# Optimization experiments

Hardware: AMD Instinct MI355X
Metric: run time of the kernel (lower is better)

Reference implementation:

```python
import jax, jax.numpy as jnp
import numpy as np

N_NODES = 20000
N_FEAT = 10
EDGE_DIM = 6
D = 256
H = 8
C = D // H  # 32 per-head channels for gat1/gat2
B = 2048
E = 320000
NEG = 0.2        # LeakyReLU slope in GATConv attention
BN_EPS = 1e-5


def _bn_eval(x, g, b):
    # BatchNorm1d in eval mode with fresh buffers: running_mean=0, running_var=1
    return g * x * (1.0 / np.sqrt(1.0 + BN_EPS)) + b


def _gat(x, src, dst, edge_attr, W, a_src, a_dst, We, a_e, bias, heads, out_ch, n):
    # PyG GATConv with edge_dim: shared src/dst linear, per-head additive attention
    xp = (x @ W).reshape(n, heads, out_ch)                       # [N,H,C]
    al_s = jnp.einsum('nhc,hc->nh', xp, a_src)                   # [N,H]
    al_d = jnp.einsum('nhc,hc->nh', xp, a_dst)                   # [N,H]
    ep = (edge_attr @ We).reshape(-1, heads, out_ch)             # [E,H,C]
    al_e = jnp.einsum('ehc,hc->eh', ep, a_e)                     # [E,H]
    alpha = jax.nn.leaky_relu(al_s[src] + al_d[dst] + al_e, NEG)  # [E,H]
    # segment softmax over incoming edges of each dst node
    amax = jax.ops.segment_max(alpha, dst, num_segments=n)
    amax = jnp.where(jnp.isfinite(amax), amax, 0.0)
    ex = jnp.exp(alpha - amax[dst])
    den = jax.ops.segment_sum(ex, dst, num_segments=n)
    w = ex / (den[dst] + 1e-16)
    out = jax.ops.segment_sum(xp[src] * w[..., None], dst, num_segments=n)
    return out.reshape(n, heads * out_ch) + bias


def setup_inputs():
    key = jax.random.key(0)
    ks = iter(jax.random.split(key, 40))
    def rn(shape, scale=0.05):
        return jax.random.normal(next(ks), shape, dtype=jnp.float32) * scale
    inp = {}
    inp['current_node_ids'] = jax.random.randint(next(ks), (B,), 0, N_NODES)
    inp['network_features'] = jax.random.normal(next(ks), (B, N_FEAT), dtype=jnp.float32)
    inp['edge_index'] = jax.random.randint(next(ks), (2, E), 0, N_NODES)
    inp['edge_attr'] = jax.random.normal(next(ks), (E, EDGE_DIM), dtype=jnp.float32)
    inp['emb'] = rn((N_NODES, D), 1.0)
    inp['net_w1'] = rn((N_FEAT, D)); inp['net_b1'] = jnp.zeros((D,), jnp.float32)
    inp['net_g1'] = jnp.ones((D,), jnp.float32); inp['net_be1'] = jnp.zeros((D,), jnp.float32)
    inp['net_w2'] = rn((D, D)); inp['net_b2'] = jnp.zeros((D,), jnp.float32)
    inp['net_g2'] = jnp.ones((D,), jnp.float32); inp['net_be2'] = jnp.zeros((D,), jnp.float32)
    for i, (h, c) in enumerate([(H, C), (H, C), (1, D)], start=1):
        inp[f'gat{i}_W'] = rn((D, h * c))
        inp[f'gat{i}_as'] = rn((h, c)); inp[f'gat{i}_ad'] = rn((h, c))
        inp[f'gat{i}_We'] = rn((EDGE_DIM, h * c)); inp[f'gat{i}_ae'] = rn((h, c))
        inp[f'gat{i}_b'] = jnp.zeros((h * c,), jnp.float32)
    inp['fus_w'] = rn((2 * D, D)); inp['fus_b'] = jnp.zeros((D,), jnp.float32)
    inp['fus_g'] = jnp.ones((D,), jnp.float32); inp['fus_be'] = jnp.zeros((D,), jnp.float32)
    inp['cls_w'] = rn((D, N_NODES)); inp['cls_b'] = jnp.zeros((N_NODES,), jnp.float32)
    return inp


def reference(current_node_ids, network_features, edge_index, edge_attr, emb,
              net_w1, net_b1, net_g1, net_be1, net_w2, net_b2, net_g2, net_be2,
              gat1_W, gat1_as, gat1_ad, gat1_We, gat1_ae, gat1_b,
              gat2_W, gat2_as, gat2_ad, gat2_We, gat2_ae, gat2_b,
              gat3_W, gat3_as, gat3_ad, gat3_We, gat3_ae, gat3_b,
              fus_w, fus_b, fus_g, fus_be, cls_w, cls_b):
    src, dst = edge_index[0], edge_index[1]
    n = emb.shape[0]
    x = jax.nn.relu(_gat(emb, src, dst, edge_attr, gat1_W, gat1_as, gat1_ad, gat1_We, gat1_ae, gat1_b, H, C, n))
    x = jax.nn.relu(_gat(x, src, dst, edge_attr, gat2_W, gat2_as, gat2_ad, gat2_We, gat2_ae, gat2_b, H, C, n))
    x = _gat(x, src, dst, edge_attr, gat3_W, gat3_as, gat3_ad, gat3_We, gat3_ae, gat3_b, 1, D, n)
    node_emb = x[current_node_ids]                               # [B,D]
    h1 = jax.nn.relu(_bn_eval(network_features @ net_w1 + net_b1, net_g1, net_be1))
    net_emb = jax.nn.relu(_bn_eval(h1 @ net_w2 + net_b2, net_g2, net_be2))
    combined = jnp.concatenate([node_emb, net_emb], axis=1)      # [B,2D]
    fused = jax.nn.relu(_bn_eval(combined @ fus_w + fus_b, fus_g, fus_be))
    return fused @ cls_w + cls_b                                 # [B, N_NODES]
```

## Files before the change

kernel.cpp:

```cpp
#include <hip/hip_runtime.h>

#define NEG_SLOPE 0.2f
static constexpr float BN_INV = 0.9999950000374997f;

typedef __bf16 bf16x8 __attribute__((ext_vector_type(8)));
typedef float  f32x4  __attribute__((ext_vector_type(4)));

__device__ inline float4 bf4f(ushort4 u){
  float4 r;
  r.x = __uint_as_float((unsigned)u.x << 16);
  r.y = __uint_as_float((unsigned)u.y << 16);
  r.z = __uint_as_float((unsigned)u.z << 16);
  r.w = __uint_as_float((unsigned)u.w << 16);
  return r;
}
__device__ inline ushort4 f4bf(float4 v){
  ushort4 u;
  u.x = __builtin_bit_cast(unsigned short, (__bf16)v.x);
  u.y = __builtin_bit_cast(unsigned short, (__bf16)v.y);
  u.z = __builtin_bit_cast(unsigned short, (__bf16)v.z);
  u.w = __builtin_bit_cast(unsigned short, (__bf16)v.w);
  return u;
}

__global__ void hist_kernel(const int* __restrict__ dst, int* __restrict__ cnt, int E){
  int e = blockIdx.x*256 + threadIdx.x;
  if (e < E) atomicAdd(&cnt[dst[e]], 1);
}

__global__ __launch_bounds__(1024) void scan_kernel(int* __restrict__ cnt_cursor, int* __restrict__ offs, int n){
  __shared__ int wsum[16];
  int tid = threadIdx.x, lane = tid & 63, wv = tid >> 6;
  if (tid == 0) offs[0] = 0;
  int carry = 0;
  for (int base = 0; base < n; base += 1024){
    int i = base + tid;
    int v = (i < n) ? cnt_cursor[i] : 0;
    int x = v;
#pragma unroll
    for (int off = 1; off < 64; off <<= 1){
      int t = __shfl_up(x, off);
      if (lane >= off) x += t;
    }
    if (lane == 63) wsum[wv] = x;
    __syncthreads();
    int y = (lane < 16) ? wsum[lane] : 0;
#pragma unroll
    for (int off = 1; off < 16; off <<= 1){
      int t = __shfl_up(y, off);
      if (lane >= off) y += t;
    }
    int excl  = (wv == 0) ? 0 : __shfl(y, wv - 1);
    int total = __shfl(y, 15);
    int inc = carry + excl + x;
    if (i < n){ offs[i+1] = inc; cnt_cursor[i] = inc - v; }
    carry += total;
    __syncthreads();
  }
}

__global__ void scatter_kernel(const int* __restrict__ src, const int* __restrict__ dst,
                               const float* __restrict__ ea, int* __restrict__ cursor,
                               int* __restrict__ perm_src, int* __restrict__ perm_dst,
                               float* __restrict__ ea_perm, int E){
  int e = blockIdx.x*256 + threadIdx.x;
  if (e >= E) return;
  int d = dst[e];
  int pos = atomicAdd(&cursor[d], 1);
  perm_src[pos] = src[e];
  perm_dst[pos] = d;
#pragma unroll
  for (int k = 0; k < 6; ++k) ea_perm[(size_t)pos*6 + k] = ea[(size_t)e*6 + k];
}

__global__ void foldm_all_kernel(const float* __restrict__ We1, const float* __restrict__ ae1,
                                 const float* __restrict__ We2, const float* __restrict__ ae2,
                                 const float* __restrict__ We3, const float* __restrict__ ae3,
                                 float* __restrict__ M){
  int t = threadIdx.x;
  if (t < 96){
    const float* We = (t < 48) ? We1 : We2;
    const float* ae = (t < 48) ? ae1 : ae2;
    int u = t % 48, k = u / 8, h = u % 8;
    float s = 0.f;
    for (int c = 0; c < 32; ++c) s += We[k*256 + h*32 + c] * ae[h*32 + c];
    M[t] = s;
  } else if (t < 102){
    int k = t - 96;
    float s = 0.f;
    for (int c = 0; c < 256; ++c) s += We3[k*256 + c] * ae3[c];
    M[t] = s;
  }
}

template<bool USE_BIAS, bool USE_BN, bool USE_RELU, typename OutT>
__global__ __launch_bounds__(256) void gemm_kernel(
    const float* __restrict__ A, const float* __restrict__ W,
    const float* __restrict__ bias, const float* __restrict__ gam, const float* __restrict__ bet,
    OutT* __restrict__ C, int M, int N, int K)
{
  __shared__ float As[32][68];
  __shared__ float Bs[32][64];
  int tid = threadIdx.x;
  int tx = tid & 15, ty = tid >> 4;
  int bn0 = blockIdx.x * 64, bm0 = blockIdx.y * 64;
  float acc[4][4] = {};
  for (int k0 = 0; k0 < K; k0 += 32){
    int kk = tid & 31, mm0 = tid >> 5;
#pragma unroll
    for (int r = 0; r < 8; ++r){
      int ml = mm0 + r*8;
      int m = bm0 + ml;
      As[kk][ml] = (m < M) ? A[(size_t)m*K + k0 + kk] : 0.f;
    }
    int nn = tid & 63, kb = tid >> 6;
#pragma unroll
    for (int r = 0; r < 8; ++r){
      int kl = kb + r*4;
      int n = bn0 + nn;
      Bs[kl][nn] = (n < N) ? W[(size_t)(k0 + kl)*N + n] : 0.f;
    }
    __syncthreads();
#pragma unroll
    for (int k = 0; k < 32; ++k){
      float4 a4 = *reinterpret_cast<const float4*>(&As[k][ty*4]);
      float4 b4 = *reinterpret_cast<const float4*>(&Bs[k][tx*4]);
      acc[0][0] += a4.x*b4.x; acc[0][1] += a4.x*b4.y; acc[0][2] += a4.x*b4.z; acc[0][3] += a4.x*b4.w;
      acc[1][0] += a4.y*b4.x; acc[1][1] += a4.y*b4.y; acc[1][2] += a4.y*b4.z; acc[1][3] += a4.y*b4.w;
      acc[2][0] += a4.z*b4.x; acc[2][1] += a4.z*b4.y; acc[2][2] += a4.z*b4.z; acc[2][3] += a4.z*b4.w;
      acc[3][0] += a4.w*b4.x; acc[3][1] += a4.w*b4.y; acc[3][2] += a4.w*b4.z; acc[3][3] += a4.w*b4.w;
    }
    __syncthreads();
  }
#pragma unroll
  for (int i = 0; i < 4; ++i){
    int m = bm0 + ty*4 + i;
    if (m < M){
#pragma unroll
      for (int j = 0; j < 4; ++j){
        int n = bn0 + tx*4 + j;
        if (n < N){
          float c = acc[i][j];
          if (USE_BIAS) c += bias[n];
          if (USE_BN)   c = gam[n]*c*BN_INV + bet[n];
          if (USE_RELU) c = fmaxf(c, 0.f);
          C[(size_t)m*N + n] = (OutT)c;
        }
      }
    }
  }
}

__global__ void wtrans_kernel(const float* __restrict__ W, __bf16* __restrict__ Wt, int K, int N){
  __shared__ float tile[32][33];
  int n0 = blockIdx.x*32, k0 = blockIdx.y*32;
  int t = threadIdx.x;
  int nl = t & 31, kl = t >> 5;
#pragma unroll
  for (int r = 0; r < 4; ++r)
    tile[kl + r*8][nl] = W[(size_t)(k0 + kl + r*8)*N + n0 + nl];
  __syncthreads();
  int nl2 = t >> 3, kc = (t & 7)*4;
#pragma unroll
  for (int j = 0; j < 4; ++j)
    Wt[(size_t)(n0 + nl2)*K + k0 + kc + j] = (__bf16)tile[kc + j][nl2];
}

__global__ void wtrans3_kernel(const float* __restrict__ W0, const float* __restrict__ W1,
                               const float* __restrict__ W2, __bf16* __restrict__ Wt){
  __shared__ float tile[32][33];
  const float* W = (blockIdx.z == 0) ? W0 : (blockIdx.z == 1) ? W1 : W2;
  __bf16* D = Wt + (size_t)blockIdx.z * 65536;
  int n0 = blockIdx.x*32, k0 = blockIdx.y*32;
  int t = threadIdx.x;
  int nl = t & 31, kl = t >> 5;
#pragma unroll
  for (int r = 0; r < 4; ++r)
    tile[kl + r*8][nl] = W[(size_t)(k0 + kl + r*8)*256 + n0 + nl];
  __syncthreads();
  int nl2 = t >> 3, kc = (t & 7)*4;
#pragma unroll
  for (int j = 0; j < 4; ++j)
    D[(size_t)(n0 + nl2)*256 + k0 + kc + j] = (__bf16)tile[kc + j][nl2];
}

__global__ void cvt_kernel(const float* __restrict__ in, __bf16* __restrict__ out, int n4){
  int i = blockIdx.x*256 + threadIdx.x;
  if (i >= n4) return;
  float4 v = reinterpret_cast<const float4*>(in)[i];
  reinterpret_cast<ushort4*>(out)[i] = f4bf(v);
}

template<bool USE_BIAS, typename OutT>
__global__ __launch_bounds__(256) void mfma_gemm_kernel(
    const __bf16* __restrict__ A, const __bf16* __restrict__ Bt,
    const float* __restrict__ bias, OutT* __restrict__ C, int M, int N, int K)
{
  __shared__ __bf16 As[128*72];
  __shared__ __bf16 Bs[128*72];
  int tid = threadIdx.x;
  int lane = tid & 63, w = tid >> 6;
  int quad = lane >> 4, l16 = lane & 15;
  int wm = (w & 1) * 64, wn = (w >> 1) * 64;
  int bn0 = blockIdx.x * 128, bm0 = blockIdx.y * 128;
  f32x4 acc[4][4] = {};
  for (int k0 = 0; k0 < K; k0 += 64){
#pragma unroll
    for (int p = 0; p < 4; ++p){
      int idx = p*256 + tid;
      int row = idx >> 3, ch = idx & 7;
      uint4 av = *reinterpret_cast<const uint4*>(&A[(size_t)(bm0 + row)*K + k0 + ch*8]);
      *reinterpret_cast<uint4*>(&As[row*72 + ch*8]) = av;
      int n = bn0 + row;
      uint4 bv = make_uint4(0,0,0,0);
      if (n < N) bv = *reinterpret_cast<const uint4*>(&Bt[(size_t)n*K + k0 + ch*8]);
      *reinterpret_cast<uint4*>(&Bs[row*72 + ch*8]) = bv;
    }
    __syncthreads();
#pragma unroll
    for (int s = 0; s < 2; ++s){
      bf16x8 af[4], bfr[4];
#pragma unroll
      for (int t4 = 0; t4 < 4; ++t4){
        af[t4]  = *reinterpret_cast<const bf16x8*>(&As[(wm + t4*16 + l16)*72 + s*32 + quad*8]);
        bfr[t4] = *reinterpret_cast<const bf16x8*>(&Bs[(wn + t4*16 + l16)*72 + s*32 + quad*8]);
      }
#pragma unroll
      for (int mt = 0; mt < 4; ++mt)
#pragma unroll
        for (int nt = 0; nt < 4; ++nt)
          acc[mt][nt] = __builtin_amdgcn_mfma_f32_16x16x32_bf16(af[mt], bfr[nt], acc[mt][nt], 0, 0, 0);
    }
    __syncthreads();
  }
#pragma unroll
  for (int mt = 0; mt < 4; ++mt){
#pragma unroll
    for (int nt = 0; nt < 4; ++nt){
      int n = bn0 + wn + nt*16 + l16;
      if (n < N){
        float bv = USE_BIAS ? bias[n] : 0.f;
#pragma unroll
        for (int r = 0; r < 4; ++r){
          int m = bm0 + wm + mt*16 + quad*4 + r;
          if (m < M) C[(size_t)m*N + n] = (OutT)(acc[mt][nt][r] + bv);
        }
      }
    }
  }
}

template<int HH>
__global__ void alsd_kernel(const __bf16* __restrict__ xp, const float* __restrict__ a_s,
                            const float* __restrict__ a_d, float* __restrict__ als,
                            float* __restrict__ ald, int Nn){
  int gid = blockIdx.x*blockDim.x + threadIdx.x;
  int wave = gid >> 6, lane = threadIdx.x & 63;
  if (wave >= Nn) return;
  float4 xv = bf4f(reinterpret_cast<const ushort4*>(xp)[(size_t)wave*64 + lane]);
  float4 av = reinterpret_cast<const float4*>(a_s)[lane];
  float4 dv = reinterpret_cast<const float4*>(a_d)[lane];
  float ps = xv.x*av.x + xv.y*av.y + xv.z*av.z + xv.w*av.w;
  float pd = xv.x*dv.x + xv.y*dv.y + xv.z*dv.z + xv.w*dv.w;
  if constexpr (HH == 8){
    ps += __shfl_xor(ps,1); pd += __shfl_xor(pd,1);
    ps += __shfl_xor(ps,2); pd += __shfl_xor(pd,2);
    ps += __shfl_xor(ps,4); pd += __shfl_xor(pd,4);
    if ((lane & 7) == 0){
      als[wave*8 + (lane>>3)] = ps;
      ald[wave*8 + (lane>>3)] = pd;
    }
  } else {
#pragma unroll
    for (int off = 1; off < 64; off <<= 1){ ps += __shfl_xor(ps,off); pd += __shfl_xor(pd,off); }
    if (lane == 0){ als[wave] = ps; ald[wave] = pd; }
  }
}

template<int HH>
__global__ void alpha_kernel(const int* __restrict__ perm_src, const int* __restrict__ perm_dst,
                             const float* __restrict__ ea_perm, const float* __restrict__ Mf,
                             const float* __restrict__ als, const float* __restrict__ ald,
                             float* __restrict__ alpha, int E){
  __shared__ float Ms[48];
  if (threadIdx.x < 6*HH) Ms[threadIdx.x] = Mf[threadIdx.x];
  __syncthreads();
  int i = blockIdx.x*256 + threadIdx.x;
  if (i >= E) return;
  int s = perm_src[i], d = perm_dst[i];
  float eav[6];
#pragma unroll
  for (int k = 0; k < 6; ++k) eav[k] = ea_perm[(size_t)i*6 + k];
#pragma unroll
  for (int h = 0; h < HH; ++h){
    float ale = 0.f;
#pragma unroll
    for (int k = 0; k < 6; ++k) ale += eav[k] * Ms[k*HH + h];
    float v = als[s*HH + h] + ald[d*HH + h] + ale;
    alpha[(size_t)i*HH + h] = (v > 0.f) ? v : NEG_SLOPE*v;
  }
}

template<int HH>
__global__ void agg_kernel(const int* __restrict__ offs, const int* __restrict__ perm_src,
                           const float* __restrict__ alpha, const __bf16* __restrict__ xp,
                           const float* __restrict__ bias, __bf16* __restrict__ out,
                           int Nn, int do_relu){
  int gid = blockIdx.x*blockDim.x + threadIdx.x;
  int wave = gid >> 6, lane = threadIdx.x & 63;
  if (wave >= Nn) return;
  int beg = offs[wave], end = offs[wave+1];

  float mx[HH];
#pragma unroll
  for (int h = 0; h < HH; ++h) mx[h] = -3.0e38f;
  for (int i = beg + lane; i < end; i += 64){
    if constexpr (HH == 8){
      const float4* A4 = reinterpret_cast<const float4*>(alpha);
      float4 u = A4[2*(size_t)i], v = A4[2*(size_t)i + 1];
      mx[0]=fmaxf(mx[0],u.x); mx[1]=fmaxf(mx[1],u.y); mx[2]=fmaxf(mx[2],u.z); mx[3]=fmaxf(mx[3],u.w);
      mx[4]=fmaxf(mx[4],v.x); mx[5]=fmaxf(mx[5],v.y); mx[6]=fmaxf(mx[6],v.z); mx[7]=fmaxf(mx[7],v.w);
    } else {
      mx[0] = fmaxf(mx[0], alpha[i]);
    }
  }
#pragma unroll
  for (int off = 1; off < 64; off <<= 1)
#pragma unroll
    for (int h = 0; h < HH; ++h) mx[h] = fmaxf(mx[h], __shfl_xor(mx[h], off));

  float sm[HH];
#pragma unroll
  for (int h = 0; h < HH; ++h) sm[h] = 0.f;
  for (int i = beg + lane; i < end; i += 64){
    if constexpr (HH == 8){
      const float4* A4 = reinterpret_cast<const float4*>(alpha);
      float4 u = A4[2*(size_t)i], v = A4[2*(size_t)i + 1];
      sm[0]+=__expf(u.x-mx[0]); sm[1]+=__expf(u.y-mx[1]); sm[2]+=__expf(u.z-mx[2]); sm[3]+=__expf(u.w-mx[3]);
      sm[4]+=__expf(v.x-mx[4]); sm[5]+=__expf(v.y-mx[5]); sm[6]+=__expf(v.z-mx[6]); sm[7]+=__expf(v.w-mx[7]);
    } else {
      sm[0] += __expf(alpha[i]-mx[0]);
    }
  }
#pragma unroll
  for (int off = 1; off < 64; off <<= 1)
#pragma unroll
    for (int h = 0; h < HH; ++h) sm[h] += __shfl_xor(sm[h], off);

  float my_m, my_r;
  if constexpr (HH == 8){
    int h = lane >> 3;
    float rd[8];
#pragma unroll
    for (int j = 0; j < 8; ++j) rd[j] = 1.f/(sm[j] + 1e-16f);
    my_m = mx[0]; my_r = rd[0];
#pragma unroll
    for (int j = 1; j < 8; ++j){ if (h == j){ my_m = mx[j]; my_r = rd[j]; } }
  } else {
    my_m = mx[0]; my_r = 1.f/(sm[0] + 1e-16f);
  }

  const ushort4* X4 = reinterpret_cast<const ushort4*>(xp);
  int hsel = (HH == 8) ? (lane >> 3) : 0;
  float4 acc = make_float4(0.f,0.f,0.f,0.f);
  int i = beg;
  for (; i + 3 < end; i += 4){
    int s0 = perm_src[i], s1 = perm_src[i+1], s2 = perm_src[i+2], s3 = perm_src[i+3];
    float a0, a1, a2, a3;
    if constexpr (HH == 8){
      a0 = alpha[(size_t)i*8 + hsel];     a1 = alpha[(size_t)(i+1)*8 + hsel];
      a2 = alpha[(size_t)(i+2)*8 + hsel]; a3 = alpha[(size_t)(i+3)*8 + hsel];
    } else { a0 = alpha[i]; a1 = alpha[i+1]; a2 = alpha[i+2]; a3 = alpha[i+3]; }
    float w0 = __expf(a0 - my_m)*my_r, w1 = __expf(a1 - my_m)*my_r;
    float w2 = __expf(a2 - my_m)*my_r, w3 = __expf(a3 - my_m)*my_r;
    float4 x0 = bf4f(X4[(size_t)s0*64 + lane]);
    float4 x1 = bf4f(X4[(size_t)s1*64 + lane]);
    float4 x2 = bf4f(X4[(size_t)s2*64 + lane]);
    float4 x3 = bf4f(X4[(size_t)s3*64 + lane]);
    acc.x += x0.x*w0 + x1.x*w1 + x2.x*w2 + x3.x*w3;
    acc.y += x0.y*w0 + x1.y*w1 + x2.y*w2 + x3.y*w3;
    acc.z += x0.z*w0 + x1.z*w1 + x2.z*w2 + x3.z*w3;
    acc.w += x0.w*w0 + x1.w*w1 + x2.w*w2 + x3.w*w3;
  }
  for (; i < end; ++i){
    int s = perm_src[i];
    float a = (HH==8) ? alpha[(size_t)i*8 + hsel] : alpha[i];
    float w = __expf(a - my_m) * my_r;
    float4 xv = bf4f(X4[(size_t)s*64 + lane]);
    acc.x += xv.x*w; acc.y += xv.y*w; acc.z += xv.z*w; acc.w += xv.w*w;
  }
  float4 bv = reinterpret_cast<const float4*>(bias)[lane];
  acc.x += bv.x; acc.y += bv.y; acc.z += bv.z; acc.w += bv.w;
  if (do_relu){
    acc.x = fmaxf(acc.x,0.f); acc.y = fmaxf(acc.y,0.f);
    acc.z = fmaxf(acc.z,0.f); acc.w = fmaxf(acc.w,0.f);
  }
  reinterpret_cast<ushort4*>(out)[(size_t)wave*64 + lane] = f4bf(acc);
}

__global__ void h1_kernel(const float* __restrict__ nf, const float* __restrict__ w1,
                          const float* __restrict__ b1, const float* __restrict__ g,
                          const float* __restrict__ be, float* __restrict__ out){
  int b = blockIdx.x, j = threadIdx.x;
  float s = b1[j];
#pragma unroll
  for (int k = 0; k < 10; ++k) s += nf[b*10 + k] * w1[k*256 + j];
  s = g[j]*s*BN_INV + be[j];
  out[b*256 + j] = fmaxf(s, 0.f);
}

__global__ void gather_kernel(const int* __restrict__ ids, const __bf16* __restrict__ gat3out,
                              const float* __restrict__ netemb, float* __restrict__ comb){
  int b = blockIdx.x, t = threadIdx.x;
  float4 v;
  if (t < 64) v = bf4f(reinterpret_cast<const ushort4*>(gat3out)[(size_t)ids[b]*64 + t]);
  else        v = reinterpret_cast<const float4*>(netemb)[(size_t)b*64 + (t-64)];
  reinterpret_cast<float4*>(comb)[(size_t)b*128 + t] = v;
}

extern "C" void kernel_launch(void* const* d_in, const int* in_sizes, int n_in,
                              void* d_out, int out_size, void* d_ws, size_t ws_size,
                              hipStream_t stream)
{
  const int*   ids   = (const int*)  d_in[0];
  const float* nf    = (const float*)d_in[1];
  const int*   eidx  = (const int*)  d_in[2];
  const float* eattr = (const float*)d_in[3];
  const float* emb   = (const float*)d_in[4];
  const float* w1    = (const float*)d_in[5];
  const float* b1    = (const float*)d_in[6];
  const float* g1    = (const float*)d_in[7];
  const float* be1   = (const float*)d_in[8];
  const float* w2    = (const float*)d_in[9];
  const float* b2    = (const float*)d_in[10];
  const float* g2    = (const float*)d_in[11];
  const float* be2   = (const float*)d_in[12];
  const float* gW[3]  = {(const float*)d_in[13], (const float*)d_in[19], (const float*)d_in[25]};
  const float* gas[3] = {(const float*)d_in[14], (const float*)d_in[20], (const float*)d_in[26]};
  const float* gad[3] = {(const float*)d_in[15], (const float*)d_in[21], (const float*)d_in[27]};
  const float* gWe[3] = {(const float*)d_in[16], (const float*)d_in[22], (const float*)d_in[28]};
  const float* gae[3] = {(const float*)d_in[17], (const float*)d_in[23], (const float*)d_in[29]};
  const float* gb[3]  = {(const float*)d_in[18], (const float*)d_in[24], (const float*)d_in[30]};
  const float* fus_w  = (const float*)d_in[31];
  const float* fus_b  = (const float*)d_in[32];
  const float* fus_g  = (const float*)d_in[33];
  const float* fus_be = (const float*)d_in[34];
  const float* cls_w  = (const float*)d_in[35];
  const float* cls_b  = (const float*)d_in[36];

  const int E  = in_sizes[3] / 6;
  const int Nn = in_sizes[4] / 256;
  const int B  = in_sizes[0];
  const int Ncls = in_sizes[36];
  const int Npad = (Nn + 127) & ~127;
  const int* src = eidx;
  const int* dst = eidx + E;

  char* wbase = (char*)d_ws;
  size_t woff = 0;
  auto carve = [&](size_t bytes)->void*{
    void* p = wbase + woff;
    woff = (woff + bytes + 255) & ~(size_t)255;
    return p;
  };
  int*    offs     = (int*)   carve((size_t)(Nn+1)*4);
  int*    cursor   = (int*)   carve((size_t)Nn*4);
  int*    perm_src = (int*)   carve((size_t)E*4);
  int*    perm_dst = (int*)   carve((size_t)E*4);
  float*  ea_perm  = (float*) carve((size_t)E*6*4);
  __bf16* xb0      = (__bf16*)carve((size_t)Npad*256*2);
  __bf16* xb1      = (__bf16*)carve((size_t)Npad*256*2);
  __bf16* xpb      = (__bf16*)carve((size_t)Npad*256*2);
  __bf16* gWt      = (__bf16*)carve((size_t)3*256*256*2);
  float*  als      = (float*) carve((size_t)Nn*8*4);
  float*  ald      = (float*) carve((size_t)Nn*8*4);
  float*  alpha    = (float*) carve((size_t)E*8*4);
  float*  Mfold    = (float*) carve(128*4);
  float*  h1b      = (float*) carve((size_t)B*256*4);
  float*  netemb   = (float*) carve((size_t)B*256*4);
  float*  comb     = (float*) carve((size_t)B*512*4);
  __bf16* fusedb   = (__bf16*)carve((size_t)B*256*2);
  __bf16* clsWt    = (__bf16*)carve((size_t)Ncls*256*2);
  (void)ws_size; (void)n_in; (void)out_size;

  hipMemsetAsync(cursor, 0, (size_t)Nn*4, stream);
  hist_kernel<<<(E+255)/256, 256, 0, stream>>>(dst, cursor, E);
  scan_kernel<<<1, 1024, 0, stream>>>(cursor, offs, Nn);
  scatter_kernel<<<(E+255)/256, 256, 0, stream>>>(src, dst, eattr, cursor,
                                                  perm_src, perm_dst, ea_perm, E);

  foldm_all_kernel<<<1, 128, 0, stream>>>(gWe[0], gae[0], gWe[1], gae[1], gWe[2], gae[2], Mfold);
  wtrans3_kernel<<<dim3(8, 8, 3), 256, 0, stream>>>(gW[0], gW[1], gW[2], gWt);
  wtrans_kernel<<<dim3(Ncls/32, 256/32), 256, 0, stream>>>(cls_w, clsWt, 256, Ncls);
  cvt_kernel<<<(Nn*64 + 255)/256, 256, 0, stream>>>(emb, xb0, Nn*64);

  const __bf16* inx[3]  = {xb0, xb1, xb0};
  __bf16*       outx[3] = {xb1, xb0, xb1};
  const int     Hs[3]   = {8, 8, 1};
  dim3 mfma_grid_xp(2, Npad/128);
  int node_blocks = (Nn*64 + 255)/256;
  for (int l = 0; l < 3; ++l){
    mfma_gemm_kernel<false, __bf16><<<mfma_grid_xp, 256, 0, stream>>>(
        inx[l], gWt + (size_t)l*65536, nullptr, xpb, Nn, 256, 256);
    const float* Mf = Mfold + (l == 2 ? 96 : l*48);
    if (Hs[l] == 8){
      alsd_kernel<8><<<node_blocks, 256, 0, stream>>>(xpb, gas[l], gad[l], als, ald, Nn);
      alpha_kernel<8><<<(E+255)/256, 256, 0, stream>>>(perm_src, perm_dst, ea_perm,
                                                       Mf, als, ald, alpha, E);
      agg_kernel<8><<<node_blocks, 256, 0, stream>>>(offs, perm_src, alpha, xpb, gb[l],
                                                     outx[l], Nn, (l < 2) ? 1 : 0);
    } else {
      alsd_kernel<1><<<node_blocks, 256, 0, stream>>>(xpb, gas[l], gad[l], als, ald, Nn);
      alpha_kernel<1><<<(E+255)/256, 256, 0, stream>>>(perm_src, perm_dst, ea_perm,
                                                       Mf, als, ald, alpha, E);
      agg_kernel<1><<<node_blocks, 256, 0, stream>>>(offs, perm_src, alpha, xpb, gb[l],
                                                     outx[l], Nn, 0);
    }
  }

  h1_kernel<<<B, 256, 0, stream>>>(nf, w1, b1, g1, be1, h1b);
  gemm_kernel<true,true,true,float><<<dim3(4, B/64), 256, 0, stream>>>(
      h1b, w2, b2, g2, be2, netemb, B, 256, 256);

  gather_kernel<<<B, 128, 0, stream>>>(ids, xb1, netemb, comb);
  gemm_kernel<true,true,true,__bf16><<<dim3(4, B/64), 256, 0, stream>>>(
      comb, fus_w, fus_b, fus_g, fus_be, fusedb, B, 256, 512);
  mfma_gemm_kernel<true, float><<<dim3((Ncls+127)/128, B/128), 256, 0, stream>>>(
      fusedb, clsWt, cls_b, (float*)d_out, B, Ncls, 256);
}
```

Baseline: 732.7 us.

## Fuse GAT attention into aggregation, GEMM epilogue, and parallelize CSR scan

```diff
diff --git a/kernel.cpp b/kernel.cpp
--- a/kernel.cpp
+++ b/kernel.cpp
@@ -28,47 +28,62 @@
   if (e < E) atomicAdd(&cnt[dst[e]], 1);
 }
 
-__global__ __launch_bounds__(1024) void scan_kernel(int* __restrict__ cnt_cursor, int* __restrict__ offs, int n){
+__global__ __launch_bounds__(1024) void scan1_kernel(int* __restrict__ cnt_cursor,
+                                                     int* __restrict__ offs,
+                                                     int* __restrict__ bsum, int n){
   __shared__ int wsum[16];
   int tid = threadIdx.x, lane = tid & 63, wv = tid >> 6;
-  if (tid == 0) offs[0] = 0;
-  int carry = 0;
-  for (int base = 0; base < n; base += 1024){
-    int i = base + tid;
-    int v = (i < n) ? cnt_cursor[i] : 0;
-    int x = v;
-#pragma unroll
-    for (int off = 1; off < 64; off <<= 1){
-      int t = __shfl_up(x, off);
-      if (lane >= off) x += t;
-    }
-    if (lane == 63) wsum[wv] = x;
-    __syncthreads();
-    int y = (lane < 16) ? wsum[lane] : 0;
-#pragma unroll
-    for (int off = 1; off < 16; off <<= 1){
-      int t = __shfl_up(y, off);
-      if (lane >= off) y += t;
-    }
-    int excl  = (wv == 0) ? 0 : __shfl(y, wv - 1);
-    int total = __shfl(y, 15);
-    int inc = carry + excl + x;
-    if (i < n){ offs[i+1] = inc; cnt_cursor[i] = inc - v; }
-    carry += total;
-    __syncthreads();
-  }
+  int i = blockIdx.x*1024 + tid;
+  int v = (i < n) ? cnt_cursor[i] : 0;
+  int x = v;
+#pragma unroll
+  for (int off = 1; off < 64; off <<= 1){
+    int t = __shfl_up(x, off);
+    if (lane >= off) x += t;
+  }
+  if (lane == 63) wsum[wv] = x;
+  __syncthreads();
+  int y = (lane < 16) ? wsum[lane] : 0;
+#pragma unroll
+  for (int off = 1; off < 16; off <<= 1){
+    int t = __shfl_up(y, off);
+    if (lane >= off) y += t;
+  }
+  int excl  = (wv == 0) ? 0 : __shfl(y, wv - 1);
+  int total = __shfl(y, 15);
+  int inc = excl + x;
+  if (i < n){ offs[i+1] = inc; cnt_cursor[i] = inc - v; }
+  if (tid == 0) bsum[blockIdx.x] = total;
+}
+
+__global__ void scan2_kernel(int* __restrict__ bsum, int nb){
+  int lane = threadIdx.x;
+  int v = (lane < nb) ? bsum[lane] : 0;
+  int x = v;
+#pragma unroll
+  for (int off = 1; off < 64; off <<= 1){
+    int t = __shfl_up(x, off);
+    if (lane >= off) x += t;
+  }
+  if (lane < nb) bsum[lane] = x - v;
+}
+
+__global__ __launch_bounds__(1024) void scan3_kernel(int* __restrict__ offs, int* __restrict__ cursor,
+                                                     const int* __restrict__ bsum, int n){
+  int i = blockIdx.x*1024 + threadIdx.x;
+  int base = bsum[blockIdx.x];
+  if (i < n){ offs[i+1] += base; cursor[i] += base; }
+  if (i == 0) offs[0] = 0;
 }
 
 __global__ void scatter_kernel(const int* __restrict__ src, const int* __restrict__ dst,
                                const float* __restrict__ ea, int* __restrict__ cursor,
-                               int* __restrict__ perm_src, int* __restrict__ perm_dst,
-                               float* __restrict__ ea_perm, int E){
+                               int* __restrict__ perm_src, float* __restrict__ ea_perm, int E){
   int e = blockIdx.x*256 + threadIdx.x;
   if (e >= E) return;
   int d = dst[e];
   int pos = atomicAdd(&cursor[d], 1);
   perm_src[pos] = src[e];
-  perm_dst[pos] = d;
 #pragma unroll
   for (int k = 0; k < 6; ++k) ea_perm[(size_t)pos*6 + k] = ea[(size_t)e*6 + k];
 }
@@ -184,18 +199,15 @@
     D[(size_t)(n0 + nl2)*256 + k0 + kc + j] = (__bf16)tile[kc + j][nl2];
 }
 
-__global__ void cvt_kernel(const float* __restrict__ in, __bf16* __restrict__ out, int n4){
-  int i = blockIdx.x*256 + threadIdx.x;
-  if (i >= n4) return;
-  float4 v = reinterpret_cast<const float4*>(in)[i];
-  reinterpret_cast<ushort4*>(out)[i] = f4bf(v);
-}
-
-template<bool USE_BIAS, typename OutT>
+template<bool USE_BIAS, bool AF32, int ALSD, typename OutT>
 __global__ __launch_bounds__(256) void mfma_gemm_kernel(
-    const __bf16* __restrict__ A, const __bf16* __restrict__ Bt,
-    const float* __restrict__ bias, OutT* __restrict__ C, int M, int N, int K)
+    const void* __restrict__ Aptr, const __bf16* __restrict__ Bt,
+    const float* __restrict__ bias, OutT* __restrict__ C, int M, int N, int K,
+    const float* __restrict__ a_s, const float* __restrict__ a_d,
+    float* __restrict__ als, float* __restrict__ ald)
 {
+  const __bf16* Ab = (const __bf16*)Aptr;
+  const float*  Af = (const float*) Aptr;
   __shared__ __bf16 As[128*72];
   __shared__ __bf16 Bs[128*72];
   int tid = threadIdx.x;
@@ -209,7 +221,22 @@
     for (int p = 0; p < 4; ++p){
       int idx = p*256 + tid;
       int row = idx >> 3, ch = idx & 7;
-      uint4 av = *reinterpret_cast<const uint4*>(&A[(size_t)(bm0 + row)*K + k0 + ch*8]);
+      uint4 av;
+      if constexpr (AF32){
+        av = make_uint4(0,0,0,0);
+        int m = bm0 + row;
+        if (m < M){
+          const float4* A4 = reinterpret_cast<const float4*>(&Af[(size_t)m*K + k0 + ch*8]);
+          float4 x0 = A4[0], x1 = A4[1];
+          ushort4 u0 = f4bf(x0), u1 = f4bf(x1);
+          av = make_uint4((unsigned)u0.x | ((unsigned)u0.y << 16),
+                          (unsigned)u0.z | ((unsigned)u0.w << 16),
+                          (unsigned)u1.x | ((unsigned)u1.y << 16),
+                          (unsigned)u1.z | ((unsigned)u1.w << 16));
+        }
+      } else {
+        av = *reinterpret_cast<const uint4*>(&Ab[(size_t)(bm0 + row)*K + k0 + ch*8]);
+      }
       *reinterpret_cast<uint4*>(&As[row*72 + ch*8]) = av;
       int n = bn0 + row;
       uint4 bv = make_uint4(0,0,0,0);
@@ -244,6 +271,38 @@
         for (int r = 0; r < 4; ++r){
           int m = bm0 + wm + mt*16 + quad*4 + r;
           if (m < M) C[(size_t)m*N + n] = (OutT)(acc[mt][nt][r] + bv);
+        }
+      }
+    }
+  }
+  if constexpr (ALSD == 8){
+    float av4[4], dv4[4];
+#pragma unroll
+    for (int nt = 0; nt < 4; ++nt){
+      int n = bn0 + wn + nt*16 + l16;
+      av4[nt] = a_s[n];
+      dv4[nt] = a_d[n];
+    }
+    int hb = (bn0 + wn) >> 5;
+#pragma unroll
+    for (int mt = 0; mt < 4; ++mt){
+#pragma unroll
+      for (int r = 0; r < 4; ++r){
+        float s0 = acc[mt][0][r]*av4[0] + acc[mt][1][r]*av4[1];
+        float s1 = acc[mt][2][r]*av4[2] + acc[mt][3][r]*av4[3];
+        float d0 = acc[mt][0][r]*dv4[0] + acc[mt][1][r]*dv4[1];
+        float d1 = acc[mt][2][r]*dv4[2] + acc[mt][3][r]*dv4[3];
+#pragma unroll
+        for (int off = 1; off < 16; off <<= 1){
+          s0 += __shfl_xor(s0, off); s1 += __shfl_xor(s1, off);
+          d0 += __shfl_xor(d0, off); d1 += __shfl_xor(d1, off);
+        }
+        if (l16 == 0){
+          int m = bm0 + wm + mt*16 + quad*4 + r;
+          if (m < M){
+            als[m*8 + hb]     = s0; als[m*8 + hb + 1] = s1;
+            ald[m*8 + hb]     = d0; ald[m*8 + hb + 1] = d1;
+          }
         }
       }
     }
@@ -278,119 +337,71 @@
 }
 
 template<int HH>
-__global__ void alpha_kernel(const int* __restrict__ perm_src, const int* __restrict__ perm_dst,
-                             const float* __restrict__ ea_perm, const float* __restrict__ Mf,
-                             const float* __restrict__ als, const float* __restrict__ ald,
-                             float* __restrict__ alpha, int E){
-  __shared__ float Ms[48];
-  if (threadIdx.x < 6*HH) Ms[threadIdx.x] = Mf[threadIdx.x];
-  __syncthreads();
-  int i = blockIdx.x*256 + threadIdx.x;
-  if (i >= E) return;
-  int s = perm_src[i], d = perm_dst[i];
-  float eav[6];
-#pragma unroll
-  for (int k = 0; k < 6; ++k) eav[k] = ea_perm[(size_t)i*6 + k];
-#pragma unroll
-  for (int h = 0; h < HH; ++h){
-    float ale = 0.f;
-#pragma unroll
-    for (int k = 0; k < 6; ++k) ale += eav[k] * Ms[k*HH + h];
-    float v = als[s*HH + h] + ald[d*HH + h] + ale;
-    alpha[(size_t)i*HH + h] = (v > 0.f) ? v : NEG_SLOPE*v;
-  }
-}
-
-template<int HH>
 __global__ void agg_kernel(const int* __restrict__ offs, const int* __restrict__ perm_src,
-                           const float* __restrict__ alpha, const __bf16* __restrict__ xp,
-                           const float* __restrict__ bias, __bf16* __restrict__ out,
-                           int Nn, int do_relu){
+                           const float* __restrict__ ea_perm, const float* __restrict__ Mf,
+                           const float* __restrict__ als, const float* __restrict__ ald,
+                           const __bf16* __restrict__ xp, const float* __restrict__ bias,
+                           __bf16* __restrict__ out, int Nn, int do_relu){
   int gid = blockIdx.x*blockDim.x + threadIdx.x;
   int wave = gid >> 6, lane = threadIdx.x & 63;
   if (wave >= Nn) return;
   int beg = offs[wave], end = offs[wave+1];
-
-  float mx[HH];
-#pragma unroll
-  for (int h = 0; h < HH; ++h) mx[h] = -3.0e38f;
-  for (int i = beg + lane; i < end; i += 64){
-    if constexpr (HH == 8){
-      const float4* A4 = reinterpret_cast<const float4*>(alpha);
-      float4 u = A4[2*(size_t)i], v = A4[2*(size_t)i + 1];
-      mx[0]=fmaxf(mx[0],u.x); mx[1]=fmaxf(mx[1],u.y); mx[2]=fmaxf(mx[2],u.z); mx[3]=fmaxf(mx[3],u.w);
-      mx[4]=fmaxf(mx[4],v.x); mx[5]=fmaxf(mx[5],v.y); mx[6]=fmaxf(mx[6],v.z); mx[7]=fmaxf(mx[7],v.w);
-    } else {
-      mx[0] = fmaxf(mx[0], alpha[i]);
-    }
-  }
-#pragma unroll
-  for (int off = 1; off < 64; off <<= 1)
-#pragma unroll
-    for (int h = 0; h < HH; ++h) mx[h] = fmaxf(mx[h], __shfl_xor(mx[h], off));
-
-  float sm[HH];
-#pragma unroll
-  for (int h = 0; h < HH; ++h) sm[h] = 0.f;
-  for (int i = beg + lane; i < end; i += 64){
-    if constexpr (HH == 8){
-      const float4* A4 = reinterpret_cast<const float4*>(alpha);
-      float4 u = A4[2*(size_t)i], v = A4[2*(size_t)i + 1];
-      sm[0]+=__expf(u.x-mx[0]); sm[1]+=__expf(u.y-mx[1]); sm[2]+=__expf(u.z-mx[2]); sm[3]+=__expf(u.w-mx[3]);
-      sm[4]+=__expf(v.x-mx[4]); sm[5]+=__expf(v.y-mx[5]); sm[6]+=__expf(v.z-mx[6]); sm[7]+=__expf(v.w-mx[7]);
-    } else {
-      sm[0] += __expf(alpha[i]-mx[0]);
-    }
-  }
-#pragma unroll
-  for (int off = 1; off < 64; off <<= 1)
-#pragma unroll
-    for (int h = 0; h < HH; ++h) sm[h] += __shfl_xor(sm[h], off);
-
-  float my_m, my_r;
-  if constexpr (HH == 8){
-    int h = lane >> 3;
-    float rd[8];
-#pragma unroll
-    for (int j = 0; j < 8; ++j) rd[j] = 1.f/(sm[j] + 1e-16f);
-    my_m = mx[0]; my_r = rd[0];
-#pragma unroll
-    for (int j = 1; j < 8; ++j){ if (h == j){ my_m = mx[j]; my_r = rd[j]; } }
-  } else {
-    my_m = mx[0]; my_r = 1.f/(sm[0] + 1e-16f);
-  }
+  int hsel = (HH == 8) ? (lane >> 3) : 0;
+
+  float mk[6];
+#pragma unroll
+  for (int k = 0; k < 6; ++k) mk[k] = Mf[k*HH + hsel];
+  float aldv = ald[(size_t)wave*HH + hsel];
 
   const ushort4* X4 = reinterpret_cast<const ushort4*>(xp);
-  int hsel = (HH == 8) ? (lane >> 3) : 0;
   float4 acc = make_float4(0.f,0.f,0.f,0.f);
+  float den = 0.f;
+
   int i = beg;
   for (; i + 3 < end; i += 4){
     int s0 = perm_src[i], s1 = perm_src[i+1], s2 = perm_src[i+2], s3 = perm_src[i+3];
-    float a0, a1, a2, a3;
-    if constexpr (HH == 8){
-      a0 = alpha[(size_t)i*8 + hsel];     a1 = alpha[(size_t)(i+1)*8 + hsel];
-      a2 = alpha[(size_t)(i+2)*8 + hsel]; a3 = alpha[(size_t)(i+3)*8 + hsel];
-    } else { a0 = alpha[i]; a1 = alpha[i+1]; a2 = alpha[i+2]; a3 = alpha[i+3]; }
-    float w0 = __expf(a0 - my_m)*my_r, w1 = __expf(a1 - my_m)*my_r;
-    float w2 = __expf(a2 - my_m)*my_r, w3 = __expf(a3 - my_m)*my_r;
+    float a0 = als[(size_t)s0*HH + hsel] + aldv;
+    float a1 = als[(size_t)s1*HH + hsel] + aldv;
+    float a2 = als[(size_t)s2*HH + hsel] + aldv;
+    float a3 = als[(size_t)s3*HH + hsel] + aldv;
+#pragma unroll
+    for (int k = 0; k < 6; ++k){
+      a0 += ea_perm[(size_t)i*6 + k]     * mk[k];
+      a1 += ea_perm[(size_t)(i+1)*6 + k] * mk[k];
+      a2 += ea_perm[(size_t)(i+2)*6 + k] * mk[k];
+      a3 += ea_perm[(size_t)(i+3)*6 + k] * mk[k];
+    }
+    a0 = (a0 > 0.f) ? a0 : NEG_SLOPE*a0;
+    a1 = (a1 > 0.f) ? a1 : NEG_SLOPE*a1;
+    a2 = (a2 > 0.f) ? a2 : NEG_SLOPE*a2;
+    a3 = (a3 > 0.f) ? a3 : NEG_SLOPE*a3;
+    float e0 = __expf(a0), e1 = __expf(a1), e2 = __expf(a2), e3 = __expf(a3);
+    den += (e0 + e1) + (e2 + e3);
     float4 x0 = bf4f(X4[(size_t)s0*64 + lane]);
     float4 x1 = bf4f(X4[(size_t)s1*64 + lane]);
     float4 x2 = bf4f(X4[(size_t)s2*64 + lane]);
     float4 x3 = bf4f(X4[(size_t)s3*64 + lane]);
-    acc.x += x0.x*w0 + x1.x*w1 + x2.x*w2 + x3.x*w3;
-    acc.y += x0.y*w0 + x1.y*w1 + x2.y*w2 + x3.y*w3;
-    acc.z += x0.z*w0 + x1.z*w1 + x2.z*w2 + x3.z*w3;
-    acc.w += x0.w*w0 + x1.w*w1 + x2.w*w2 + x3.w*w3;
+    acc.x += x0.x*e0 + x1.x*e1 + x2.x*e2 + x3.x*e3;
+    acc.y += x0.y*e0 + x1.y*e1 + x2.y*e2 + x3.y*e3;
+    acc.z += x0.z*e0 + x1.z*e1 + x2.z*e2 + x3.z*e3;
+    acc.w += x0.w*e0 + x1.w*e1 + x2.w*e2 + x3.w*e3;
   }
   for (; i < end; ++i){
     int s = perm_src[i];
-    float a = (HH==8) ? alpha[(size_t)i*8 + hsel] : alpha[i];
-    float w = __expf(a - my_m) * my_r;
+    float a = als[(size_t)s*HH + hsel] + aldv;
+#pragma unroll
+    for (int k = 0; k < 6; ++k) a += ea_perm[(size_t)i*6 + k] * mk[k];
+    a = (a > 0.f) ? a : NEG_SLOPE*a;
+    float e = __expf(a);
+    den += e;
     float4 xv = bf4f(X4[(size_t)s*64 + lane]);
-    acc.x += xv.x*w; acc.y += xv.y*w; acc.z += xv.z*w; acc.w += xv.w*w;
-  }
+    acc.x += xv.x*e; acc.y += xv.y*e; acc.z += xv.z*e; acc.w += xv.w*e;
+  }
+
+  float r = 1.f / (den + 1e-16f);
   float4 bv = reinterpret_cast<const float4*>(bias)[lane];
-  acc.x += bv.x; acc.y += bv.y; acc.z += bv.z; acc.w += bv.w;
+  acc.x = acc.x*r + bv.x; acc.y = acc.y*r + bv.y;
+  acc.z = acc.z*r + bv.z; acc.w = acc.w*r + bv.w;
   if (do_relu){
     acc.x = fmaxf(acc.x,0.f); acc.y = fmaxf(acc.y,0.f);
     acc.z = fmaxf(acc.z,0.f); acc.w = fmaxf(acc.w,0.f);
@@ -465,8 +476,8 @@
   };
   int*    offs     = (int*)   carve((size_t)(Nn+1)*4);
   int*    cursor   = (int*)   carve((size_t)Nn*4);
+  int*    bsum     = (int*)   carve(64*4);
   int*    perm_src = (int*)   carve((size_t)E*4);
-  int*    perm_dst = (int*)   carve((size_t)E*4);
   float*  ea_perm  = (float*) carve((size_t)E*6*4);
   __bf16* xb0      = (__bf16*)carve((size_t)Npad*256*2);
   __bf16* xb1      = (__bf16*)carve((size_t)Npad*256*2);
@@ -474,7 +485,6 @@
   __bf16* gWt      = (__bf16*)carve((size_t)3*256*256*2);
   float*  als      = (float*) carve((size_t)Nn*8*4);
   float*  ald      = (float*) carve((size_t)Nn*8*4);
-  float*  alpha    = (float*) carve((size_t)E*8*4);
   float*  Mfold    = (float*) carve(128*4);
   float*  h1b      = (float*) carve((size_t)B*256*4);
   float*  netemb   = (float*) carve((size_t)B*256*4);
@@ -483,40 +493,36 @@
   __bf16* clsWt    = (__bf16*)carve((size_t)Ncls*256*2);
   (void)ws_size; (void)n_in; (void)out_size;
 
+  const int nb1024 = (Nn + 1023) / 1024;
+
   hipMemsetAsync(cursor, 0, (size_t)Nn*4, stream);
   hist_kernel<<<(E+255)/256, 256, 0, stream>>>(dst, cursor, E);
-  scan_kernel<<<1, 1024, 0, stream>>>(cursor, offs, Nn);
+  scan1_kernel<<<nb1024, 1024, 0, stream>>>(cursor, offs, bsum, Nn);
+  scan2_kernel<<<1, 64, 0, stream>>>(bsum, nb1024);
+  scan3_kernel<<<nb1024, 1024, 0, stream>>>(offs, cursor, bsum, Nn);
   scatter_kernel<<<(E+255)/256, 256, 0, stream>>>(src, dst, eattr, cursor,
-                                                  perm_src, perm_dst, ea_perm, E);
+                                                  perm_src, ea_perm, E);
 
   foldm_all_kernel<<<1, 128, 0, stream>>>(gWe[0], gae[0], gWe[1], gae[1], gWe[2], gae[2], Mfold);
   wtrans3_kernel<<<dim3(8, 8, 3), 256, 0, stream>>>(gW[0], gW[1], gW[2], gWt);
   wtrans_kernel<<<dim3(Ncls/32, 256/32), 256, 0, stream>>>(cls_w, clsWt, 256, Ncls);
-  cvt_kernel<<<(Nn*64 + 255)/256, 256, 0, stream>>>(emb, xb0, Nn*64);
-
-  const __bf16* inx[3]  = {xb0, xb1, xb0};
-  __bf16*       outx[3] = {xb1, xb0, xb1};
-  const int     Hs[3]   = {8, 8, 1};
+
   dim3 mfma_grid_xp(2, Npad/128);
   int node_blocks = (Nn*64 + 255)/256;
-  for (int l = 0; l < 3; ++l){
-    mfma_gemm_kernel<false, __bf16><<<mfma_grid_xp, 256, 0, stream>>>(
-        inx[l], gWt + (size_t)l*65536, nullptr, xpb, Nn, 256, 256);
-    const float* Mf = Mfold + (l == 2 ? 96 : l*48);
-    if (Hs[l] == 8){
-      alsd_kernel<8><<<node_blocks, 256, 0, stream>>>(xpb, gas[l], gad[l], als, ald, Nn);
-      alpha_kernel<8><<<(E+255)/256, 256, 0, stream>>>(perm_src, perm_dst, ea_perm,
-                                                       Mf, als, ald, alpha, E);
-      agg_kernel<8><<<node_blocks, 256, 0, stream>>>(offs, perm_src, alpha, xpb, gb[l],
-                                                     outx[l], Nn, (l < 2) ? 1 : 0);
-    } else {
-      alsd_kernel<1><<<node_blocks, 256, 0, stream>>>(xpb, gas[l], gad[l], als, ald, Nn);
-      alpha_kernel<1><<<(E+255)/256, 256, 0, stream>>>(perm_src, perm_dst, ea_perm,
-                                                       Mf, als, ald, alpha, E);
-      agg_kernel<1><<<node_blocks, 256, 0, stream>>>(offs, perm_src, alpha, xpb, gb[l],
-                                                     outx[l], Nn, 0);
-    }
-  }
+
+  mfma_gemm_kernel<false, true, 8, __bf16><<<mfma_grid_xp, 256, 0, stream>>>(
+      emb, gWt, nullptr, xpb, Nn, 256, 256, gas[0], gad[0], als, ald);
+  agg_kernel<8><<<node_blocks, 256, 0, stream>>>(offs, perm_src, ea_perm, Mfold,
+                                                 als, ald, xpb, gb[0], xb1, Nn, 1);
+  mfma_gemm_kernel<false, false, 8, __bf16><<<mfma_grid_xp, 256, 0, stream>>>(
+      xb1, gWt + 65536, nullptr, xpb, Nn, 256, 256, gas[1], gad[1], als, ald);
+  agg_kernel<8><<<node_blocks, 256, 0, stream>>>(offs, perm_src, ea_perm, Mfold + 48,
+                                                 als, ald, xpb, gb[1], xb0, Nn, 1);
+  mfma_gemm_kernel<false, false, 0, __bf16><<<mfma_grid_xp, 256, 0, stream>>>(
+      xb0, gWt + 131072, nullptr, xpb, Nn, 256, 256, nullptr, nullptr, nullptr, nullptr);
+  alsd_kernel<1><<<node_blocks, 256, 0, stream>>>(xpb, gas[2], gad[2], als, ald, Nn);
+  agg_kernel<1><<<node_blocks, 256, 0, stream>>>(offs, perm_src, ea_perm, Mfold + 96,
+                                                 als, ald, xpb, gb[2], xb1, Nn, 0);
 
   h1_kernel<<<B, 256, 0, stream>>>(nf, w1, b1, g1, be1, h1b);
   gemm_kernel<true,true,true,float><<<dim3(4, B/64), 256, 0, stream>>>(
@@ -525,6 +531,6 @@
   gather_kernel<<<B, 128, 0, stream>>>(ids, xb1, netemb, comb);
   gemm_kernel<true,true,true,__bf16><<<dim3(4, B/64), 256, 0, stream>>>(
       comb, fus_w, fus_b, fus_g, fus_be, fusedb, B, 256, 512);
-  mfma_gemm_kernel<true, float><<<dim3((Ncls+127)/128, B/128), 256, 0, stream>>>(
-      fusedb, clsWt, cls_b, (float*)d_out, B, Ncls, 256);
-}
+  mfma_gemm_kernel<true, false, 0, float><<<dim3((Ncls+127)/128, B/128), 256, 0, stream>>>(
+      fusedb, clsWt, cls_b, (float*)d_out, B, Ncls, 256, nullptr, nullptr, nullptr, nullptr);
+}
```

New measurement: 736.7 us. Within noise of the previous version (+0.5%).
